# Kernel optimization log

Measured on AMD Instinct MI355X. Metric: run time of the kernel, lower is better.

## Reference

```python
import jax, jax.numpy as jnp
import numpy as np

B, L, N, D = 32, 32, 8, 256
A = 16          # action_dim
AENC = 32       # action_enc_dim (hardcoded in module)
EFF = 32        # effect_dim (hardcoded in module)


def _lin(k, din, dout):
    return jax.random.normal(k, (din, dout), jnp.float32) * 0.02, jnp.zeros((dout,), jnp.float32)


def _mlp(x, w1, b1, w2, b2, act):
    # two-layer torch Sequential: Linear -> ELU -> Linear -> act
    return act(jax.nn.elu(x @ w1 + b1) @ w2 + b2)


_SPECS = [
    ("in_",  D,        D, D),    # inertia_encoder (final ELU)
    ("ae_",  A,        D, AENC), # action_encoder (final ELU)
    ("eff_", D + AENC, D, D),    # action_effect_network (final ELU)
    ("aat_", D + AENC, D, 1),    # action_attn_network (final Sigmoid)
    ("pw_",  2 * D, 2 * D, D),   # pairwise_encoder (final ELU)
    ("ie_",  D,        D, EFF),  # interaction_effect_network (final ELU)
    ("ia_",  D,        D, 1),    # interaction_attn_network (final Sigmoid)
    ("fm_",  D + EFF,  D, D),    # final_merge_network (final ELU)
    ("out_", D,        D, D),    # output_network (no final act)
]


def setup_inputs() -> dict:
    key = jax.random.key(0)
    ks = jax.random.split(key, 2 + len(_SPECS))
    inp = {
        "samples": jax.random.normal(ks[0], (B, L, N, D), jnp.float32),
        "action": jax.random.randint(ks[1], (B, L), 0, A),
        "mask": jnp.ones((B, L), jnp.bool_),
    }
    for i, (p, d0, dh, d1) in enumerate(_SPECS):
        k1, k2 = jax.random.split(ks[2 + i])
        inp[p + "w1"], inp[p + "b1"] = _lin(k1, d0, dh)
        inp[p + "w2"], inp[p + "b2"] = _lin(k2, dh, d1)
    return inp


def _forward(samples, action,
             in_w1, in_b1, in_w2, in_b2,
             ae_w1, ae_b1, ae_w2, ae_b2,
             eff_w1, eff_b1, eff_w2, eff_b2,
             aat_w1, aat_b1, aat_w2, aat_b2,
             pw_w1, pw_b1, pw_w2, pw_b2,
             ie_w1, ie_b1, ie_w2, ie_b2,
             ia_w1, ia_b1, ia_w2, ia_b2,
             fm_w1, fm_b1, fm_w2, fm_b2,
             out_w1, out_b1, out_w2, out_b2):
    elu, sig = jax.nn.elu, jax.nn.sigmoid
    ident = lambda x: x
    b, l, n, d = samples.shape

    act_oh = jax.nn.one_hot(action, A, dtype=jnp.float32)          # (B,L,A)
    state = _mlp(samples, in_w1, in_b1, in_w2, in_b2, elu)          # (B,L,N,D)
    aenc = _mlp(act_oh, ae_w1, ae_b1, ae_w2, ae_b2, elu)            # (B,L,AENC)
    aenc = jnp.broadcast_to(aenc[:, :, None, :], (b, l, n, AENC))   # same action per slot

    sa = jnp.concatenate([state, aenc], axis=-1)                    # (B,L,N,D+AENC)
    s_eff = _mlp(sa, eff_w1, eff_b1, eff_w2, eff_b2, elu)           # (B,L,N,D)
    s_att = _mlp(sa, aat_w1, aat_b1, aat_w2, aat_b2, sig)           # (B,L,N,1)
    state_enc = s_eff * s_att                                       # (B,L,N,D)

    # all ordered pairs (i, j!=i), matching the torch double loop
    jidx = np.array([[j for j in range(n) if j != i] for i in range(n)])  # (N,N-1)
    src = jnp.broadcast_to(state_enc[:, :, :, None, :], (b, l, n, n - 1, d))
    tgt = state_enc[:, :, jidx, :]                                  # (B,L,N,N-1,D)
    pairs = jnp.concatenate([src, tgt], axis=-1)                    # (B,L,N,N-1,2D)

    pint = _mlp(pairs, pw_w1, pw_b1, pw_w2, pw_b2, elu)             # (B,L,N,N-1,D)
    p_eff = _mlp(pint, ie_w1, ie_b1, ie_w2, ie_b2, elu)             # (B,L,N,N-1,EFF)
    p_att = _mlp(pint, ia_w1, ia_b1, ia_w2, ia_b2, sig)             # (B,L,N,N-1,1)
    total_effect = jnp.sum(p_eff * p_att, axis=3)                   # (B,L,N,EFF)

    merged = _mlp(jnp.concatenate([state_enc, total_effect], axis=-1),
                  fm_w1, fm_b1, fm_w2, fm_b2, elu)                  # (B,L,N,D)
    return _mlp(merged, out_w1, out_b1, out_w2, out_b2, ident)      # (B,L,N,D)


def reference(samples, action, mask,
              in_w1, in_b1, in_w2, in_b2,
              ae_w1, ae_b1, ae_w2, ae_b2,
              eff_w1, eff_b1, eff_w2, eff_b2,
              aat_w1, aat_b1, aat_w2, aat_b2,
              pw_w1, pw_b1, pw_w2, pw_b2,
              ie_w1, ie_b1, ie_w2, ie_b2,
              ia_w1, ia_b1, ia_w2, ia_b2,
              fm_w1, fm_b1, fm_w2, fm_b2,
              out_w1, out_b1, out_w2, out_b2):
    # mask is accepted but unused, as in the original forward
    return _forward(samples, action,
                    in_w1, in_b1, in_w2, in_b2,
                    ae_w1, ae_b1, ae_w2, ae_b2,
                    eff_w1, eff_b1, eff_w2, eff_b2,
                    aat_w1, aat_b1, aat_w2, aat_b2,
                    pw_w1, pw_b1, pw_w2, pw_b2,
                    ie_w1, ie_b1, ie_w2, ie_b2,
                    ia_w1, ia_b1, ia_w2, ia_b2,
                    fm_w1, fm_b1, fm_w2, fm_b2,
                    out_w1, out_b1, out_w2, out_b2)
```

## Files before the change

### kernel.cpp

```cpp
#include <hip/hip_runtime.h>
#include <math.h>


#define BLN 8192
#define BL  1024

__device__ __forceinline__ float eluf(float x)  { return x > 0.0f ? x : expm1f(x); }
__device__ __forceinline__ float sigmf_(float x){ return 1.0f / (1.0f + expf(-x)); }

template<int ACT, bool ROWSCALE, bool PAIRGATHER>
__global__ __launch_bounds__(256) void gemm_k(
    const float* __restrict__ A, int lda,
    const float* __restrict__ W, int ldw,
    const float* __restrict__ bias,
    float* __restrict__ C, int ldc,
    int K,
    const float* __restrict__ rowscale,
    const float* __restrict__ Vm, int jj)
{
  __shared__ float As[32][68];
  __shared__ float Ws[32][64];
  const int m0 = blockIdx.x * 64;
  const int n0 = blockIdx.y * 64;
  const int tid = threadIdx.x;

  const int arow = tid >> 2;
  const int akg  = (tid & 3) << 3;
  const int wrow = tid >> 3;
  const int wcg  = (tid & 7) << 3;

  const int tr = (tid >> 4) << 2;
  const int tc = (tid & 15) << 2;

  const int gr = m0 + arow;
  const float* aptr;
  const float* vptr = nullptr;
  if (PAIRGATHER) {
    const int i = gr & 7;
    const int j = jj + ((jj >= i) ? 1 : 0);
    const int vr = (gr & ~7) | j;
    aptr = A  + (size_t)gr * lda + akg;
    vptr = Vm + (size_t)vr * lda + akg;
  } else {
    aptr = A + (size_t)gr * lda + akg;
  }
  const float* wptr = W + (size_t)wrow * ldw + n0 + wcg;

  float acc[4][4] = {};

  for (int k0 = 0; k0 < K; k0 += 32) {
    float av[8];
    if (PAIRGATHER) {
      float4 u0 = *(const float4*)(aptr + k0);
      float4 u1 = *(const float4*)(aptr + k0 + 4);
      float4 v0 = *(const float4*)(vptr + k0);
      float4 v1 = *(const float4*)(vptr + k0 + 4);
      av[0]=eluf(u0.x+v0.x); av[1]=eluf(u0.y+v0.y); av[2]=eluf(u0.z+v0.z); av[3]=eluf(u0.w+v0.w);
      av[4]=eluf(u1.x+v1.x); av[5]=eluf(u1.y+v1.y); av[6]=eluf(u1.z+v1.z); av[7]=eluf(u1.w+v1.w);
    } else {
      float4 a0 = *(const float4*)(aptr + k0);
      float4 a1 = *(const float4*)(aptr + k0 + 4);
      av[0]=a0.x; av[1]=a0.y; av[2]=a0.z; av[3]=a0.w;
      av[4]=a1.x; av[5]=a1.y; av[6]=a1.z; av[7]=a1.w;
    }
    float4 w0 = *(const float4*)(wptr + (size_t)k0 * ldw);
    float4 w1 = *(const float4*)(wptr + (size_t)k0 * ldw + 4);

    __syncthreads();
#pragma unroll
    for (int i = 0; i < 8; ++i) As[akg + i][arow] = av[i];
    *(float4*)&Ws[wrow][wcg]     = w0;
    *(float4*)&Ws[wrow][wcg + 4] = w1;
    __syncthreads();

#pragma unroll
    for (int k = 0; k < 32; ++k) {
      float4 a = *(const float4*)&As[k][tr];
      float4 w = *(const float4*)&Ws[k][tc];
      acc[0][0] += a.x*w.x; acc[0][1] += a.x*w.y; acc[0][2] += a.x*w.z; acc[0][3] += a.x*w.w;
      acc[1][0] += a.y*w.x; acc[1][1] += a.y*w.y; acc[1][2] += a.y*w.z; acc[1][3] += a.y*w.w;
      acc[2][0] += a.z*w.x; acc[2][1] += a.z*w.y; acc[2][2] += a.z*w.z; acc[2][3] += a.z*w.w;
      acc[3][0] += a.w*w.x; acc[3][1] += a.w*w.y; acc[3][2] += a.w*w.z; acc[3][3] += a.w*w.w;
    }
  }

  float bv[4] = {0.f, 0.f, 0.f, 0.f};
  if (bias) {
    float4 b = *(const float4*)(bias + n0 + tc);
    bv[0]=b.x; bv[1]=b.y; bv[2]=b.z; bv[3]=b.w;
  }
#pragma unroll
  for (int i = 0; i < 4; ++i) {
    const int r = m0 + tr + i;
    float v0 = acc[i][0] + bv[0];
    float v1 = acc[i][1] + bv[1];
    float v2 = acc[i][2] + bv[2];
    float v3 = acc[i][3] + bv[3];
    if (ACT == 1) { v0=eluf(v0); v1=eluf(v1); v2=eluf(v2); v3=eluf(v3); }
    else if (ACT == 2) { v0=sigmf_(v0); v1=sigmf_(v1); v2=sigmf_(v2); v3=sigmf_(v3); }
    if (ROWSCALE) { float s = rowscale[r]; v0*=s; v1*=s; v2*=s; v3*=s; }
    float4 o; o.x=v0; o.y=v1; o.z=v2; o.w=v3;
    *(float4*)&C[(size_t)r * ldc + n0 + tc] = o;
  }
}

__global__ __launch_bounds__(256) void ae_kernel(
    const int* __restrict__ action,
    const float* __restrict__ w1, const float* __restrict__ b1,
    const float* __restrict__ w2, const float* __restrict__ b2,
    float* __restrict__ aenc)
{
  __shared__ float hs[256];
  const int bl = blockIdx.x;
  const int t = threadIdx.x;
  const int a = action[bl];
  hs[t] = eluf(w1[a * 256 + t] + b1[t]);
  __syncthreads();
  if (t < 32) {
    float acc = 0.f;
    for (int k = 0; k < 256; ++k) acc += hs[k] * w2[k * 32 + t];
    aenc[bl * 32 + t] = eluf(acc + b2[t]);
  }
}

__global__ __launch_bounds__(256) void sa_fill_kernel(const float* __restrict__ aenc,
                                                      float* __restrict__ sa2)
{
  const int idx = blockIdx.x * 256 + threadIdx.x;
  const int r = idx >> 5, c = idx & 31;
  sa2[(size_t)r * 288 + 256 + c] = aenc[(r >> 3) * 32 + c];
}

__global__ __launch_bounds__(256) void zero_teff_kernel(float* __restrict__ sa2)
{
  const int idx = blockIdx.x * 256 + threadIdx.x;
  const int r = idx >> 5, c = idx & 31;
  sa2[(size_t)r * 288 + 256 + c] = 0.f;
}

__global__ __launch_bounds__(256) void satt_kernel(
    const float* __restrict__ hea, const float* __restrict__ w,
    const float* __restrict__ b, float* __restrict__ satt)
{
  const int wv = threadIdx.x >> 6;
  const int lane = threadIdx.x & 63;
  const int row = blockIdx.x * 4 + wv;
  const float* h = hea + (size_t)row * 512 + 256;
  float acc = 0.f;
#pragma unroll
  for (int m = 0; m < 4; ++m) acc += h[lane + 64 * m] * w[lane + 64 * m];
#pragma unroll
  for (int off = 32; off; off >>= 1) acc += __shfl_xor(acc, off, 64);
  if (lane == 0) satt[row] = sigmf_(acc + b[0]);
}

__global__ __launch_bounds__(256) void pair_l2_kernel(
    const float* __restrict__ h,
    const float* __restrict__ ie_w2, const float* __restrict__ ie_b2,
    const float* __restrict__ ia_w2, const float* __restrict__ ia_b2,
    float* __restrict__ sa2)
{
  __shared__ float hs[8][512];
  __shared__ float pas[8];
  const int r0 = blockIdx.x * 8;
  const int tid = threadIdx.x;
#pragma unroll
  for (int it = 0; it < 4; ++it) {
    const int f4 = it * 256 + tid;
    const int rr = f4 >> 7;
    const int cc = (f4 & 127) << 2;
    *(float4*)&hs[rr][cc] = *(const float4*)&h[(size_t)(r0 + rr) * 512 + cc];
  }
  __syncthreads();
  const int row = tid >> 5;
  const int col = tid & 31;
  float pa = 0.f;
#pragma unroll
  for (int m = 0; m < 8; ++m) pa += hs[row][256 + col + 32 * m] * ia_w2[col + 32 * m];
#pragma unroll
  for (int off = 16; off; off >>= 1) pa += __shfl_xor(pa, off, 64);
  if (col == 0) pas[row] = sigmf_(pa + ia_b2[0]);
  float acc = 0.f;
  for (int k = 0; k < 256; ++k) acc += hs[row][k] * ie_w2[k * 32 + col];
  __syncthreads();
  const float val = eluf(acc + ie_b2[col]) * pas[row];
  sa2[(size_t)(r0 + row) * 288 + 256 + col] += val;
}

__global__ __launch_bounds__(256) void concat_w_kernel(
    const float* __restrict__ a, const float* __restrict__ b,
    float* __restrict__ dst, int N)
{
  const int idx = blockIdx.x * 256 + threadIdx.x;
  const int k = idx / (2 * N);
  const int n = idx % (2 * N);
  dst[idx] = (n < N) ? a[k * N + n] : b[k * N + (n - N)];
}

__global__ __launch_bounds__(512) void concat_b_kernel(
    const float* __restrict__ a, const float* __restrict__ b,
    float* __restrict__ dst, int N)
{
  const int t = threadIdx.x;
  dst[t] = (t < N) ? a[t] : b[t - N];
}

extern "C" void kernel_launch(void* const* d_in, const int* in_sizes, int n_in,
                              void* d_out, int out_size, void* d_ws, size_t ws_size,
                              hipStream_t stream) {
  const float* samples = (const float*)d_in[0];
  const int*   action  = (const int*)d_in[1];
  const float* in_w1  = (const float*)d_in[3];
  const float* in_b1  = (const float*)d_in[4];
  const float* in_w2  = (const float*)d_in[5];
  const float* in_b2  = (const float*)d_in[6];
  const float* ae_w1  = (const float*)d_in[7];
  const float* ae_b1  = (const float*)d_in[8];
  const float* ae_w2  = (const float*)d_in[9];
  const float* ae_b2  = (const float*)d_in[10];
  const float* eff_w1 = (const float*)d_in[11];
  const float* eff_b1 = (const float*)d_in[12];
  const float* eff_w2 = (const float*)d_in[13];
  const float* eff_b2 = (const float*)d_in[14];
  const float* aat_w1 = (const float*)d_in[15];
  const float* aat_b1 = (const float*)d_in[16];
  const float* aat_w2 = (const float*)d_in[17];
  const float* aat_b2 = (const float*)d_in[18];
  const float* pw_w1  = (const float*)d_in[19];
  const float* pw_b1  = (const float*)d_in[20];
  const float* pw_w2  = (const float*)d_in[21];
  const float* pw_b2  = (const float*)d_in[22];
  const float* ie_w1  = (const float*)d_in[23];
  const float* ie_b1  = (const float*)d_in[24];
  const float* ie_w2  = (const float*)d_in[25];
  const float* ie_b2  = (const float*)d_in[26];
  const float* ia_w1  = (const float*)d_in[27];
  const float* ia_b1  = (const float*)d_in[28];
  const float* ia_w2  = (const float*)d_in[29];
  const float* ia_b2  = (const float*)d_in[30];
  const float* fm_w1  = (const float*)d_in[31];
  const float* fm_b1  = (const float*)d_in[32];
  const float* fm_w2  = (const float*)d_in[33];
  const float* fm_b2  = (const float*)d_in[34];
  const float* out_w1 = (const float*)d_in[35];
  const float* out_b1 = (const float*)d_in[36];
  const float* out_w2 = (const float*)d_in[37];
  const float* out_b2 = (const float*)d_in[38];
  float* out = (float*)d_out;

  float* ws = (float*)d_ws;
  float* sa2     = ws;
  float* h1      = sa2     + (size_t)BLN*288;
  float* hea     = h1      + (size_t)BLN*256;
  float* U       = hea     + (size_t)BLN*512;
  float* V       = U       + (size_t)BLN*512;
  float* pint    = V       + (size_t)BLN*512;
  float* aenc    = pint    + (size_t)BLN*256;
  float* satt    = aenc    + (size_t)BL*32;
  float* wcat_ea = satt    + BLN;
  float* bcat_ea = wcat_ea + 288*512;
  float* wcat_ii = bcat_ea + 512;
  float* bcat_ii = wcat_ii + 256*512;

  const dim3 blk(256);

  concat_w_kernel<<<dim3(288*512/256), blk, 0, stream>>>(eff_w1, aat_w1, wcat_ea, 256);
  concat_b_kernel<<<dim3(1), dim3(512), 0, stream>>>(eff_b1, aat_b1, bcat_ea, 256);
  concat_w_kernel<<<dim3(256*512/256), blk, 0, stream>>>(ie_w1, ia_w1, wcat_ii, 256);
  concat_b_kernel<<<dim3(1), dim3(512), 0, stream>>>(ie_b1, ia_b1, bcat_ii, 256);

  ae_kernel<<<dim3(BL), blk, 0, stream>>>(action, ae_w1, ae_b1, ae_w2, ae_b2, aenc);

  gemm_k<1,false,false><<<dim3(128,4), blk, 0, stream>>>(samples, 256, in_w1, 256, in_b1, h1, 256, 256, nullptr, nullptr, 0);
  gemm_k<1,false,false><<<dim3(128,4), blk, 0, stream>>>(h1, 256, in_w2, 256, in_b2, sa2, 288, 256, nullptr, nullptr, 0);
  sa_fill_kernel<<<dim3(BLN*32/256), blk, 0, stream>>>(aenc, sa2);

  gemm_k<1,false,false><<<dim3(128,8), blk, 0, stream>>>(sa2, 288, wcat_ea, 512, bcat_ea, hea, 512, 288, nullptr, nullptr, 0);
  satt_kernel<<<dim3(BLN/4), blk, 0, stream>>>(hea, aat_w2, aat_b2, satt);
  gemm_k<1,true,false><<<dim3(128,4), blk, 0, stream>>>(hea, 512, eff_w2, 256, eff_b2, sa2, 288, 256, satt, nullptr, 0);

  gemm_k<0,false,false><<<dim3(128,8), blk, 0, stream>>>(sa2, 288, pw_w1, 512, pw_b1, U, 512, 256, nullptr, nullptr, 0);
  gemm_k<0,false,false><<<dim3(128,8), blk, 0, stream>>>(sa2, 288, pw_w1 + 256*512, 512, nullptr, V, 512, 256, nullptr, nullptr, 0);

  zero_teff_kernel<<<dim3(BLN*32/256), blk, 0, stream>>>(sa2);

  for (int jj = 0; jj < 7; ++jj) {
    gemm_k<1,false,true><<<dim3(128,4), blk, 0, stream>>>(U, 512, pw_w2, 256, pw_b2, pint, 256, 512, nullptr, V, jj);
    gemm_k<1,false,false><<<dim3(128,8), blk, 0, stream>>>(pint, 256, wcat_ii, 512, bcat_ii, hea, 512, 256, nullptr, nullptr, 0);
    pair_l2_kernel<<<dim3(BLN/8), blk, 0, stream>>>(hea, ie_w2, ie_b2, ia_w2, ia_b2, sa2);
  }

  gemm_k<1,false,false><<<dim3(128,4), blk, 0, stream>>>(sa2, 288, fm_w1, 256, fm_b1, h1, 256, 288, nullptr, nullptr, 0);
  gemm_k<1,false,false><<<dim3(128,4), blk, 0, stream>>>(h1, 256, fm_w2, 256, fm_b2, pint, 256, 256, nullptr, nullptr, 0);

  gemm_k<1,false,false><<<dim3(128,4), blk, 0, stream>>>(pint, 256, out_w1, 256, out_b1, h1, 256, 256, nullptr, nullptr, 0);
  gemm_k<0,false,false><<<dim3(128,4), blk, 0, stream>>>(h1, 256, out_w2, 256, out_b2, out, 256, 256, nullptr, nullptr, 0);
}
```

Measured before the change: 1.128 ms.

## Double-buffer GEMM shared tiles and batch all seven pair iterations into single launches

The GEMM kernel now uses double-buffered shared memory. The next K-tile is loaded into registers while the current tile is being computed, and the second barrier per iteration is removed. The seven per-pair-offset launches of the pairwise GEMMs and the layer-2 kernel are merged into one large-grid launch each when the workspace is big enough. A new kernel sums the interaction effects across all pairs in registers, which replaces the zeroing kernel and the read-modify-write accumulation. The batched path needs a much larger workspace (7x pint and hea buffers) and adds extra memory traffic; it falls back to the old loop otherwise.

After: 1.457 ms. +29.2%, slower.

```diff
diff --git a/kernel.cpp b/kernel.cpp
--- a/kernel.cpp
+++ b/kernel.cpp
@@ -18,8 +18,8 @@
     const float* __restrict__ rowscale,
     const float* __restrict__ Vm, int jj)
 {
-  __shared__ float As[32][68];
-  __shared__ float Ws[32][64];
+  __shared__ float As[2][32][68];
+  __shared__ float Ws[2][32][64];
   const int m0 = blockIdx.x * 64;
   const int n0 = blockIdx.y * 64;
   const int tid = threadIdx.x;
@@ -36,10 +36,12 @@
   const float* aptr;
   const float* vptr = nullptr;
   if (PAIRGATHER) {
-    const int i = gr & 7;
-    const int j = jj + ((jj >= i) ? 1 : 0);
-    const int vr = (gr & ~7) | j;
-    aptr = A  + (size_t)gr * lda + akg;
+    const int jjv = (jj >= 0) ? jj : (gr >> 13);
+    const int r = gr & (BLN - 1);
+    const int i = r & 7;
+    const int j = jjv + ((jjv >= i) ? 1 : 0);
+    const int vr = (r & ~7) | j;
+    aptr = A  + (size_t)r * lda + akg;
     vptr = Vm + (size_t)vr * lda + akg;
   } else {
     aptr = A + (size_t)gr * lda + akg;
@@ -48,46 +50,57 @@
 
   float acc[4][4] = {};
 
-  for (int k0 = 0; k0 < K; k0 += 32) {
+  float4 ra0, ra1, rv0, rv1, rw0, rw1;
+
+  auto LOAD = [&](int k0) {
+    ra0 = *(const float4*)(aptr + k0);
+    ra1 = *(const float4*)(aptr + k0 + 4);
+    if (PAIRGATHER) {
+      rv0 = *(const float4*)(vptr + k0);
+      rv1 = *(const float4*)(vptr + k0 + 4);
+    }
+    rw0 = *(const float4*)(wptr + (size_t)k0 * ldw);
+    rw1 = *(const float4*)(wptr + (size_t)k0 * ldw + 4);
+  };
+  auto STORE = [&](int buf) {
     float av[8];
     if (PAIRGATHER) {
-      float4 u0 = *(const float4*)(aptr + k0);
-      float4 u1 = *(const float4*)(aptr + k0 + 4);
-      float4 v0 = *(const float4*)(vptr + k0);
-      float4 v1 = *(const float4*)(vptr + k0 + 4);
-      av[0]=eluf(u0.x+v0.x); av[1]=eluf(u0.y+v0.y); av[2]=eluf(u0.z+v0.z); av[3]=eluf(u0.w+v0.w);
-      av[4]=eluf(u1.x+v1.x); av[5]=eluf(u1.y+v1.y); av[6]=eluf(u1.z+v1.z); av[7]=eluf(u1.w+v1.w);
+      av[0]=eluf(ra0.x+rv0.x); av[1]=eluf(ra0.y+rv0.y); av[2]=eluf(ra0.z+rv0.z); av[3]=eluf(ra0.w+rv0.w);
+      av[4]=eluf(ra1.x+rv1.x); av[5]=eluf(ra1.y+rv1.y); av[6]=eluf(ra1.z+rv1.z); av[7]=eluf(ra1.w+rv1.w);
     } else {
-      float4 a0 = *(const float4*)(aptr + k0);
-      float4 a1 = *(const float4*)(aptr + k0 + 4);
-      av[0]=a0.x; av[1]=a0.y; av[2]=a0.z; av[3]=a0.w;
-      av[4]=a1.x; av[5]=a1.y; av[6]=a1.z; av[7]=a1.w;
-    }
-    float4 w0 = *(const float4*)(wptr + (size_t)k0 * ldw);
-    float4 w1 = *(const float4*)(wptr + (size_t)k0 * ldw + 4);
-
+      av[0]=ra0.x; av[1]=ra0.y; av[2]=ra0.z; av[3]=ra0.w;
+      av[4]=ra1.x; av[5]=ra1.y; av[6]=ra1.z; av[7]=ra1.w;
+    }
+#pragma unroll
+    for (int i2 = 0; i2 < 8; ++i2) As[buf][akg + i2][arow] = av[i2];
+    *(float4*)&Ws[buf][wrow][wcg]     = rw0;
+    *(float4*)&Ws[buf][wrow][wcg + 4] = rw1;
+  };
+
+  LOAD(0);
+  STORE(0);
+  const int nt = K >> 5;
+  for (int t = 0; t < nt; ++t) {
     __syncthreads();
-#pragma unroll
-    for (int i = 0; i < 8; ++i) As[akg + i][arow] = av[i];
-    *(float4*)&Ws[wrow][wcg]     = w0;
-    *(float4*)&Ws[wrow][wcg + 4] = w1;
-    __syncthreads();
-
+    const bool more = (t + 1 < nt);
+    if (more) LOAD((t + 1) << 5);
+    const int b = t & 1;
 #pragma unroll
     for (int k = 0; k < 32; ++k) {
-      float4 a = *(const float4*)&As[k][tr];
-      float4 w = *(const float4*)&Ws[k][tc];
+      float4 a = *(const float4*)&As[b][k][tr];
+      float4 w = *(const float4*)&Ws[b][k][tc];
       acc[0][0] += a.x*w.x; acc[0][1] += a.x*w.y; acc[0][2] += a.x*w.z; acc[0][3] += a.x*w.w;
       acc[1][0] += a.y*w.x; acc[1][1] += a.y*w.y; acc[1][2] += a.y*w.z; acc[1][3] += a.y*w.w;
       acc[2][0] += a.z*w.x; acc[2][1] += a.z*w.y; acc[2][2] += a.z*w.z; acc[2][3] += a.z*w.w;
       acc[3][0] += a.w*w.x; acc[3][1] += a.w*w.y; acc[3][2] += a.w*w.z; acc[3][3] += a.w*w.w;
     }
+    if (more) STORE((t + 1) & 1);
   }
 
   float bv[4] = {0.f, 0.f, 0.f, 0.f};
   if (bias) {
-    float4 b = *(const float4*)(bias + n0 + tc);
-    bv[0]=b.x; bv[1]=b.y; bv[2]=b.z; bv[3]=b.w;
+    float4 bq = *(const float4*)(bias + n0 + tc);
+    bv[0]=bq.x; bv[1]=bq.y; bv[2]=bq.z; bv[3]=bq.w;
   }
 #pragma unroll
   for (int i = 0; i < 4; ++i) {
@@ -185,6 +198,44 @@
   __syncthreads();
   const float val = eluf(acc + ie_b2[col]) * pas[row];
   sa2[(size_t)(r0 + row) * 288 + 256 + col] += val;
+}
+
+__global__ __launch_bounds__(256) void pair_l2_all_kernel(
+    const float* __restrict__ h,
+    const float* __restrict__ ie_w2, const float* __restrict__ ie_b2,
+    const float* __restrict__ ia_w2, const float* __restrict__ ia_b2,
+    float* __restrict__ sa2)
+{
+  __shared__ float hs[8][512];
+  __shared__ float pas[8];
+  const int r0 = blockIdx.x * 8;
+  const int tid = threadIdx.x;
+  const int row = tid >> 5;
+  const int col = tid & 31;
+  float teff = 0.f;
+  for (int jj = 0; jj < 7; ++jj) {
+    __syncthreads();
+    const float* hb = h + ((size_t)jj * BLN + r0) * 512;
+#pragma unroll
+    for (int it = 0; it < 4; ++it) {
+      const int f4 = it * 256 + tid;
+      const int rr = f4 >> 7;
+      const int cc = (f4 & 127) << 2;
+      *(float4*)&hs[rr][cc] = *(const float4*)&hb[(size_t)rr * 512 + cc];
+    }
+    __syncthreads();
+    float pa = 0.f;
+#pragma unroll
+    for (int m = 0; m < 8; ++m) pa += hs[row][256 + col + 32 * m] * ia_w2[col + 32 * m];
+#pragma unroll
+    for (int off = 16; off; off >>= 1) pa += __shfl_xor(pa, off, 64);
+    if (col == 0) pas[row] = sigmf_(pa + ia_b2[0]);
+    float acc = 0.f;
+    for (int k = 0; k < 256; ++k) acc += hs[row][k] * ie_w2[k * 32 + col];
+    __syncthreads();
+    teff += eluf(acc + ie_b2[col]) * pas[row];
+  }
+  sa2[(size_t)(r0 + row) * 288 + 256 + col] = teff;
 }
 
 __global__ __launch_bounds__(256) void concat_w_kernel(
@@ -261,6 +312,11 @@
   float* bcat_ea = wcat_ea + 288*512;
   float* wcat_ii = bcat_ea + 512;
   float* bcat_ii = wcat_ii + 256*512;
+  float* arena_end = bcat_ii + 512;
+  float* pint_all = arena_end;
+  float* hea_all  = pint_all + (size_t)7*BLN*256;
+  const size_t need_batched = ((size_t)63497216) * sizeof(float);
+  const bool batched = (ws_size >= need_batched);
 
   const dim3 blk(256);
 
@@ -282,12 +338,17 @@
   gemm_k<0,false,false><<<dim3(128,8), blk, 0, stream>>>(sa2, 288, pw_w1, 512, pw_b1, U, 512, 256, nullptr, nullptr, 0);
   gemm_k<0,false,false><<<dim3(128,8), blk, 0, stream>>>(sa2, 288, pw_w1 + 256*512, 512, nullptr, V, 512, 256, nullptr, nullptr, 0);
 
-  zero_teff_kernel<<<dim3(BLN*32/256), blk, 0, stream>>>(sa2);
-
-  for (int jj = 0; jj < 7; ++jj) {
-    gemm_k<1,false,true><<<dim3(128,4), blk, 0, stream>>>(U, 512, pw_w2, 256, pw_b2, pint, 256, 512, nullptr, V, jj);
-    gemm_k<1,false,false><<<dim3(128,8), blk, 0, stream>>>(pint, 256, wcat_ii, 512, bcat_ii, hea, 512, 256, nullptr, nullptr, 0);
-    pair_l2_kernel<<<dim3(BLN/8), blk, 0, stream>>>(hea, ie_w2, ie_b2, ia_w2, ia_b2, sa2);
+  if (batched) {
+    gemm_k<1,false,true><<<dim3(128*7,4), blk, 0, stream>>>(U, 512, pw_w2, 256, pw_b2, pint_all, 256, 512, nullptr, V, -1);
+    gemm_k<1,false,false><<<dim3(128*7,8), blk, 0, stream>>>(pint_all, 256, wcat_ii, 512, bcat_ii, hea_all, 512, 256, nullptr, nullptr, 0);
+    pair_l2_all_kernel<<<dim3(BLN/8), blk, 0, stream>>>(hea_all, ie_w2, ie_b2, ia_w2, ia_b2, sa2);
+  } else {
+    zero_teff_kernel<<<dim3(BLN*32/256), blk, 0, stream>>>(sa2);
+    for (int jj = 0; jj < 7; ++jj) {
+      gemm_k<1,false,true><<<dim3(128,4), blk, 0, stream>>>(U, 512, pw_w2, 256, pw_b2, pint, 256, 512, nullptr, V, jj);
+      gemm_k<1,false,false><<<dim3(128,8), blk, 0, stream>>>(pint, 256, wcat_ii, 512, bcat_ii, hea, 512, 256, nullptr, nullptr, 0);
+      pair_l2_kernel<<<dim3(BLN/8), blk, 0, stream>>>(hea, ie_w2, ie_b2, ia_w2, ia_b2, sa2);
+    }
   }
 
   gemm_k<1,false,false><<<dim3(128,4), blk, 0, stream>>>(sa2, 288, fm_w1, 256, fm_b1, h1, 256, 288, nullptr, nullptr, 0);
```
